# Performance work log

Hardware: AMD Instinct MI355X
Metric: run time of the kernel (lower is better)

Reference implementation:

```python
import jax, jax.numpy as jnp
import numpy as np

H = 8        # heads
DK = 64      # dim_key
L = 64       # rel_pos_length
BN_EPS = 1e-5


def calc_reindexing_tensor(l, Lr):
    # Appendix B (5): band indicator of shape [l, l, 2L-1]
    x = jnp.arange(l)[:, None, None]
    i = jnp.arange(l)[None, :, None]
    r = jnp.arange(-(Lr - 1), Lr)[None, None, :]
    return ((i - x == r) & (jnp.abs(i - x) <= Lr)).astype(jnp.float32)


def setup_inputs() -> dict:
    key = jax.random.key(0)
    ks = jax.random.split(key, 6)
    b, c, x, y = 8, 256, 64, 64
    dim_hidden = H * DK
    return {
        "img": jax.random.normal(ks[0], (b, c, x, y), jnp.float32),
        "w_qkv": jax.random.normal(ks[1], (dim_hidden * 3, c), jnp.float32) * 0.02,
        "w_out": jax.random.normal(ks[2], (c, dim_hidden), jnp.float32) * 0.02,
        "b_out": jnp.zeros((c,), jnp.float32),
        "rel_rows": jax.random.normal(ks[3], (2 * L - 1, DK), jnp.float32),
        "rel_columns": jax.random.normal(ks[4], (2 * L - 1, DK), jnp.float32),
        "bn_gamma": jnp.ones((DK,), jnp.float32),
        "bn_beta": jnp.zeros((DK,), jnp.float32),
    }


def reference(img, w_qkv, w_out, b_out, rel_rows, rel_columns, bn_gamma, bn_beta):
    b, c, x, y = img.shape
    m = x * y
    # 1x1 conv (no bias) == channel GEMM
    qkv = jnp.einsum('bcxy,oc->boxy', img, w_qkv)
    q, k, v = jnp.split(qkv, 3, axis=1)
    # (b, H*DK, x, y) -> (b*H, DK, x*y)
    q = q.reshape(b * H, DK, m)
    k = k.reshape(b * H, DK, m)
    v = v.reshape(b * H, DK, m)

    # linear-attention content path
    k = jax.nn.softmax(k, axis=-1)
    context = jnp.einsum('ndm,nem->nde', k, v)          # (n, DK, DK)
    content_out = jnp.einsum('nde,ndm->nem', context, q)  # norm_queries=False
    content_out = content_out.reshape(b * H, DK, x, y)

    # relative-position path (dense banded einsums, faithful to original)
    q4 = q.reshape(b * H, DK, x, y)
    v4 = v.reshape(b * H, DK, x, y)
    Ix = calc_reindexing_tensor(x, L)                   # (x, x, 2L-1)
    Px = jnp.einsum('xir,rd->xid', Ix, rel_rows)        # (x, x, DK)
    Sx = jnp.einsum('ndxy,xid->nixy', q4, Px)
    Yh = jnp.einsum('nixy,neiy->nexy', Sx, v4)
    # BatchNorm2d(DK), training-mode batch stats over (n, x, y)
    mean = Yh.mean(axis=(0, 2, 3), keepdims=True)
    var = Yh.var(axis=(0, 2, 3), keepdims=True)
    Yh = (Yh - mean) * jax.lax.rsqrt(var + BN_EPS)
    Yh = Yh * bn_gamma[None, :, None, None] + bn_beta[None, :, None, None]

    Iy = Ix if x == y else calc_reindexing_tensor(y, L)
    Py = jnp.einsum('yir,rd->yid', Iy, rel_columns)     # (y, y, DK)
    Sy = jnp.einsum('ndxy,yid->nixy', q4, Py)
    rel_pos_out = jnp.einsum('nixy,nexi->nexy', Sy, Yh)

    out = content_out + rel_pos_out                     # (b*H, DK, x, y)
    out = out.reshape(b, H * DK, x, y)
    # 1x1 conv with bias
    return jnp.einsum('bcxy,oc->boxy', out, w_out) + b_out[None, :, None, None]
```

## Files before the change

### kernel.cpp

```cpp
#include <hip/hip_runtime.h>
#include <hip/hip_bf16.h>
#include <math.h>

#define NH   64
#define DKC  64
#define MM   4096
#define CC   256
#define RRN  127

typedef __hip_bfloat16 bf16;
__device__ __forceinline__ float b2f(bf16 x) { return __bfloat162float(x); }
__device__ __forceinline__ bf16 f2b(float x) { return __float2bfloat16(x); }
__device__ __forceinline__ unsigned short bbits(float x) { bf16 h = f2b(x); return *(unsigned short*)&h; }
__device__ __forceinline__ float fbits(unsigned short u) { bf16 h = *(bf16*)&u; return b2f(h); }

typedef short bf16x8 __attribute__((ext_vector_type(8)));
typedef float f32x4 __attribute__((ext_vector_type(4)));
typedef unsigned short u16;
typedef u16 u16x4 __attribute__((ext_vector_type(4)));
typedef u16 u16x8 __attribute__((ext_vector_type(8)));

#define AS1 __attribute__((address_space(1)))
#define AS3 __attribute__((address_space(3)))
#define GLOAD16(gp, lp) __builtin_amdgcn_global_load_lds((const AS1 void*)(gp), (AS3 void*)(lp), 16, 0, 0)

__device__ __forceinline__ int swzsrc(int lane) { return 8 * ((lane & 7) ^ (lane >> 3)); }
#define FRSWZ(kelem, row) ((kelem) ^ (((row) & 7) * 8))

__global__ __launch_bounds__(256) void k_cvt_all(const float* __restrict__ w_qkv, const float* __restrict__ w_out,
                                                 const float* __restrict__ relc, const float* __restrict__ relr,
                                                 bf16* __restrict__ wb, bf16* __restrict__ wb2,
                                                 bf16* __restrict__ relcb, bf16* __restrict__ relrb) {
  const int i = blockIdx.x * 256 + threadIdx.x;
  if (i < 393216) {
    wb[i] = f2b(w_qkv[i]);
  } else if (i < 524288) {
    int j = i - 393216; wb2[j] = f2b(w_out[j]);
  } else if (i < 532480) {
    int j = i - 524288; relcb[j] = (j < RRN * 64) ? f2b(relc[j]) : f2b(0.f);
  } else {
    int j = i - 532480; if (j < RRN * 64) relrb[j] = f2b(relr[j]);
  }
}

__global__ __launch_bounds__(256) void k_timg(const float* __restrict__ img, bf16* __restrict__ imgT) {
  const int b = blockIdx.z, c0 = blockIdx.y * 64, m0 = blockIdx.x * 64;
  const int tid = threadIdx.x;
  __shared__ short T[64 * 66];
  const float* ib = img + ((size_t)b * CC + c0) * MM + m0;
#pragma unroll
  for (int j = 0; j < 4; ++j) {
    int f4 = j * 256 + tid;
    int cc = f4 >> 4, mm4 = (f4 & 15) * 4;
    f32x4 v = *(const f32x4*)&ib[(size_t)cc * MM + mm4];
#pragma unroll
    for (int k = 0; k < 4; ++k) T[cc * 66 + mm4 + k] = (short)bbits(v[k]);
  }
  __syncthreads();
  bf16* ob = imgT + ((size_t)b * MM + m0) * CC + c0;
#pragma unroll
  for (int j = 0; j < 4; ++j) {
    int f4 = j * 256 + tid;
    int mm = f4 >> 4, cc4 = (f4 & 15) * 4;
    u16x4 pk;
#pragma unroll
    for (int k = 0; k < 4; ++k) pk[k] = (u16)T[(cc4 + k) * 66 + mm];
    *(u16x4*)&ob[(size_t)mm * CC + cc4] = pk;
  }
}

__global__ __launch_bounds__(256) void k_qkv(const bf16* __restrict__ wb, const bf16* __restrict__ imgT,
                                             bf16* __restrict__ qT, bf16* __restrict__ kk, bf16* __restrict__ v) {
  const int bI = blockIdx.z;
  const int o0 = blockIdx.y * 128;
  const int m0 = blockIdx.x * 128;
  const int tid = threadIdx.x;
  const int lane = tid & 63, wid = tid >> 6;
  const int fr = lane & 15;
  const int fq = lane >> 4;
  const int wm = (wid >> 1) * 64, wn = (wid & 1) * 64;

  __shared__ __align__(16) short smem[17408];
  short* As = smem;
  short* Bs = smem + 8192;

  const bf16* iB = imgT + (size_t)bI * MM * CC;

  f32x4 acc[4][4];
#pragma unroll
  for (int mi = 0; mi < 4; ++mi)
#pragma unroll
    for (int ni = 0; ni < 4; ++ni) acc[mi][ni] = (f32x4){0.f, 0.f, 0.f, 0.f};

  const int srow = lane >> 3;
  const int skc = swzsrc(lane);

  for (int kt = 0; kt < 4; ++kt) {
    const int k0 = kt * 64;
#pragma unroll
    for (int cc = 0; cc < 4; ++cc) {
      const int c = wid * 4 + cc;
      const int r = c * 8 + srow;
      GLOAD16(wb + (size_t)(o0 + r) * CC + k0 + skc, &As[c * 512]);
      GLOAD16(iB + (size_t)(m0 + r) * CC + k0 + skc, &Bs[c * 512]);
    }
    __syncthreads();
    bf16x8 af[4][2], bfr[4][2];
#pragma unroll
    for (int mi = 0; mi < 4; ++mi)
#pragma unroll
      for (int kkk = 0; kkk < 2; ++kkk)
        af[mi][kkk] = *(const bf16x8*)&As[(wm + mi * 16 + fr) * 64 + FRSWZ(kkk * 32 + fq * 8, fr)];
#pragma unroll
    for (int ni = 0; ni < 4; ++ni)
#pragma unroll
      for (int kkk = 0; kkk < 2; ++kkk)
        bfr[ni][kkk] = *(const bf16x8*)&Bs[(wn + ni * 16 + fr) * 64 + FRSWZ(kkk * 32 + fq * 8, fr)];
#pragma unroll
    for (int mi = 0; mi < 4; ++mi)
#pragma unroll
      for (int ni = 0; ni < 4; ++ni)
#pragma unroll
        for (int kkk = 0; kkk < 2; ++kkk)
          acc[mi][ni] = __builtin_amdgcn_mfma_f32_16x16x32_bf16(af[mi][kkk], bfr[ni][kkk], acc[mi][ni], 0, 0, 0);
    __syncthreads();
  }

  short* Cs = smem;
  if (o0 < 512) {
#pragma unroll
    for (int mi = 0; mi < 4; ++mi)
#pragma unroll
      for (int ni = 0; ni < 4; ++ni)
#pragma unroll
        for (int r = 0; r < 4; ++r)
          Cs[(wn + ni * 16 + fr) * 136 + wm + mi * 16 + fq * 4 + r] = (short)bbits(acc[mi][ni][r]);
    __syncthreads();
    const int n0 = bI * 8 + (o0 >> 6);
#pragma unroll
    for (int j = 0; j < 8; ++j) {
      int flat = tid + j * 256;
      int m = flat >> 4, nh = (flat >> 3) & 1, ds = flat & 7;
      u16x8 pk = *(const u16x8*)&Cs[m * 136 + nh * 64 + ds * 8];
      *(u16x8*)&qT[((size_t)(n0 + nh) * MM + m0 + m) * 64 + ds * 8] = pk;
    }
  } else {
#pragma unroll
    for (int mi = 0; mi < 4; ++mi)
#pragma unroll
      for (int ni = 0; ni < 4; ++ni)
#pragma unroll
        for (int r = 0; r < 4; ++r)
          Cs[(wm + mi * 16 + fq * 4 + r) * 136 + wn + ni * 16 + fr] = (short)bbits(acc[mi][ni][r]);
    __syncthreads();
    bf16* dst = (o0 < 1024) ? kk : v;
    const int obase = (o0 < 1024) ? (o0 - 512) : (o0 - 1024);
#pragma unroll
    for (int j = 0; j < 8; ++j) {
      int flat = tid + j * 256;
      int row = flat >> 4, seg = flat & 15;
      u16x8 pk = *(const u16x8*)&Cs[row * 136 + seg * 8];
      *(u16x8*)&dst[((size_t)bI * 512 + obase + row) * MM + m0 + seg * 8] = pk;
    }
  }
}

__global__ __launch_bounds__(256) void k_softmax(bf16* __restrict__ kk) {
  const size_t row = blockIdx.x;
  bf16* p = kk + row * (size_t)MM;
  const int t = threadIdx.x;
  __shared__ float sred[4];
  float v[16];
  float mx = -1e30f;
#pragma unroll
  for (int j = 0; j < 4; ++j) {
    u16x4 v4 = *(const u16x4*)&p[(j * 256 + t) * 4];
#pragma unroll
    for (int k = 0; k < 4; ++k) { v[j * 4 + k] = fbits(v4[k]); mx = fmaxf(mx, v[j * 4 + k]); }
  }
#pragma unroll
  for (int off = 32; off; off >>= 1) mx = fmaxf(mx, __shfl_down(mx, off));
  if ((t & 63) == 0) sred[t >> 6] = mx;
  __syncthreads();
  mx = fmaxf(fmaxf(sred[0], sred[1]), fmaxf(sred[2], sred[3]));
  __syncthreads();
  float s = 0.f;
#pragma unroll
  for (int i = 0; i < 16; ++i) { v[i] = expf(v[i] - mx); s += v[i]; }
#pragma unroll
  for (int off = 32; off; off >>= 1) s += __shfl_down(s, off);
  if ((t & 63) == 0) sred[t >> 6] = s;
  __syncthreads();
  s = sred[0] + sred[1] + sred[2] + sred[3];
  const float inv = 1.0f / s;
#pragma unroll
  for (int j = 0; j < 4; ++j) {
    u16x4 o;
#pragma unroll
    for (int k = 0; k < 4; ++k) o[k] = bbits(v[j * 4 + k] * inv);
    *(u16x4*)&p[(j * 256 + t) * 4] = o;
  }
}

__global__ __launch_bounds__(256) void k_ctx2(const bf16* __restrict__ kk, const bf16* __restrict__ v,
                                              float* __restrict__ part) {
  const int ch = blockIdx.x, n = blockIdx.y;
  const int tid = threadIdx.x;
  const int lane = tid & 63, wid = tid >> 6;
  const int fr = lane & 15, fq = lane >> 4;
  const int wr = (wid >> 1) * 32, wc = (wid & 1) * 32;
  __shared__ __align__(16) short Ks[64 * 64];
  __shared__ __align__(16) short Vs[64 * 64];
  const bf16* kp = kk + (size_t)n * DKC * MM;
  const bf16* vp = v + (size_t)n * DKC * MM;
  const int srow = lane >> 3;
  const int skc = swzsrc(lane);

  f32x4 acc[2][2];
#pragma unroll
  for (int mi = 0; mi < 2; ++mi)
#pragma unroll
    for (int ni = 0; ni < 2; ++ni) acc[mi][ni] = (f32x4){0.f, 0.f, 0.f, 0.f};

  for (int t = 0; t < 16; ++t) {
    const int m0 = ch * 1024 + t * 64;
#pragma unroll
    for (int cc = 0; cc < 4; ++cc) {
      const int c = wid * 4 + cc;
      if (c < 8) {
        const int r = c * 8 + srow;
        GLOAD16(kp + (size_t)r * MM + m0 + skc, &Ks[c * 512]);
      } else {
        const int r = (c - 8) * 8 + srow;
        GLOAD16(vp + (size_t)r * MM + m0 + skc, &Vs[(c - 8) * 512]);
      }
    }
    __syncthreads();
    bf16x8 af[2][2], bf[2][2];
#pragma unroll
    for (int mi = 0; mi < 2; ++mi)
#pragma unroll
      for (int kkx = 0; kkx < 2; ++kkx)
        af[mi][kkx] = *(const bf16x8*)&Ks[(wr + mi * 16 + fr) * 64 + FRSWZ(kkx * 32 + fq * 8, fr)];
#pragma unroll
    for (int ni = 0; ni < 2; ++ni)
#pragma unroll
      for (int kkx = 0; kkx < 2; ++kkx)
        bf[ni][kkx] = *(const bf16x8*)&Vs[(wc + ni * 16 + fr) * 64 + FRSWZ(kkx * 32 + fq * 8, fr)];
#pragma unroll
    for (int mi = 0; mi < 2; ++mi)
#pragma unroll
      for (int ni = 0; ni < 2; ++ni)
#pragma unroll
        for (int kkx = 0; kkx < 2; ++kkx)
          acc[mi][ni] = __builtin_amdgcn_mfma_f32_16x16x32_bf16(af[mi][kkx], bf[ni][kkx], acc[mi][ni], 0, 0, 0);
    __syncthreads();
  }
  float* pb = part + ((size_t)ch * NH + n) * 4096;
#pragma unroll
  for (int mi = 0; mi < 2; ++mi)
#pragma unroll
    for (int ni = 0; ni < 2; ++ni)
#pragma unroll
      for (int r = 0; r < 4; ++r)
        pb[(wr + mi * 16 + fq * 4 + r) * 64 + wc + ni * 16 + fr] = acc[mi][ni][r];
}

__global__ __launch_bounds__(256) void k_ctx_red(const float* __restrict__ part, float* __restrict__ ctx) {
  const int idx = blockIdx.x * 256 + threadIdx.x;
  float s = 0.f;
#pragma unroll
  for (int c = 0; c < 4; ++c) s += part[(size_t)c * 262144 + idx];
  ctx[idx] = s;
}

__global__ __launch_bounds__(256) void k_ctxT(const float* __restrict__ ctx, bf16* __restrict__ ctxTb) {
  const int n = blockIdx.x;
  const int tid = threadIdx.x;
  __shared__ float T[64 * 67];
  const float* cn = ctx + (size_t)n * 4096;
#pragma unroll
  for (int l = 0; l < 16; ++l) {
    int idx = tid + l * 256;
    int d = idx >> 6, e = idx & 63;
    T[d * 67 + e] = cn[idx];
  }
  __syncthreads();
  bf16* ob = ctxTb + (size_t)n * 4096;
#pragma unroll
  for (int l = 0; l < 4; ++l) {
    int q = tid + l * 256;
    int e = q >> 4, d4 = (q & 15) * 4;
    u16x4 pk;
#pragma unroll
    for (int k = 0; k < 4; ++k) pk[k] = bbits(T[(d4 + k) * 67 + e]);
    *(u16x4*)&ob[e * 64 + d4] = pk;
  }
}

__global__ __launch_bounds__(256) void k_sx2(const bf16* __restrict__ relrb, const bf16* __restrict__ qT,
                                             bf16* __restrict__ sxT) {
  const int x = blockIdx.x, n = blockIdx.y;
  const int tid = threadIdx.x;
  const int lane = tid & 63, wid = tid >> 6;
  const int fr = lane & 15, fq = lane >> 4;
  const int wr = (wid >> 1) * 32, wc = (wid & 1) * 32;
  __shared__ __align__(16) short Qt[64 * 64];
  const bf16* qrow = qT + ((size_t)n * MM + x * 64) * 64;
  const int srow = lane >> 3, skc = swzsrc(lane);
#pragma unroll
  for (int cc = 0; cc < 2; ++cc) {
    const int c = wid * 2 + cc;
    const int r = c * 8 + srow;
    GLOAD16(qrow + (size_t)r * 64 + skc, &Qt[c * 512]);
  }
  bf16x8 af[2][2];
#pragma unroll
  for (int mi = 0; mi < 2; ++mi) {
    const int j = wr + mi * 16 + fr + 63 - x;
#pragma unroll
    for (int kk = 0; kk < 2; ++kk)
      af[mi][kk] = *(const bf16x8*)&relrb[(size_t)j * 64 + kk * 32 + fq * 8];
  }
  __syncthreads();
  bf16x8 bq[2][2];
#pragma unroll
  for (int ni = 0; ni < 2; ++ni) {
    const int row = wc + ni * 16 + fr;
#pragma unroll
    for (int kk = 0; kk < 2; ++kk)
      bq[ni][kk] = *(const bf16x8*)&Qt[row * 64 + FRSWZ(kk * 32 + fq * 8, fr)];
  }
  f32x4 acc[2][2];
#pragma unroll
  for (int mi = 0; mi < 2; ++mi)
#pragma unroll
    for (int ni = 0; ni < 2; ++ni) acc[mi][ni] = (f32x4){0.f, 0.f, 0.f, 0.f};
#pragma unroll
  for (int mi = 0; mi < 2; ++mi)
#pragma unroll
    for (int ni = 0; ni < 2; ++ni)
#pragma unroll
      for (int kk = 0; kk < 2; ++kk)
        acc[mi][ni] = __builtin_amdgcn_mfma_f32_16x16x32_bf16(af[mi][kk], bq[ni][kk], acc[mi][ni], 0, 0, 0);
#pragma unroll
  for (int mi = 0; mi < 2; ++mi)
#pragma unroll
    for (int ni = 0; ni < 2; ++ni) {
      const int yy2 = wc + ni * 16 + fr;
      u16x4 pk;
#pragma unroll
      for (int r = 0; r < 4; ++r) pk[r] = bbits(acc[mi][ni][r]);
      *(u16x4*)&sxT[(((size_t)n * 64 + yy2) * 64 + x) * 64 + wr + mi * 16 + fq * 4] = pk;
    }
}

__global__ __launch_bounds__(256) void k_vt(const bf16* __restrict__ v, bf16* __restrict__ vT) {
  const int eg = blockIdx.x, n = blockIdx.y;
  const int tid = threadIdx.x;
  __shared__ short T[8 * 64 * 66];
  const bf16* vp = v + (size_t)n * DKC * MM + (size_t)eg * 8 * MM;
#pragma unroll
  for (int j = 0; j < 16; ++j) {
    int flat = (j * 256 + tid) * 8;
    int e = flat >> 12, m = flat & 4095;
    int x = m >> 6, y0 = m & 63;
    u16x4 lo = *(const u16x4*)&vp[(size_t)e * MM + m];
    u16x4 hi = *(const u16x4*)&vp[(size_t)e * MM + m + 4];
#pragma unroll
    for (int k = 0; k < 4; ++k) T[(e * 64 + y0 + k) * 66 + x] = (short)lo[k];
#pragma unroll
    for (int k = 0; k < 4; ++k) T[(e * 64 + y0 + 4 + k) * 66 + x] = (short)hi[k];
  }
  __syncthreads();
#pragma unroll
  for (int j = 0; j < 32; ++j) {
    int flat4 = j * 256 + tid;
    int x4 = flat4 & 15, e = (flat4 >> 4) & 7, y = flat4 >> 7;
    u16x4 pk;
#pragma unroll
    for (int r = 0; r < 4; ++r) pk[r] = (u16)T[(e * 64 + y) * 66 + x4 * 4 + r];
    *(u16x4*)&vT[(((size_t)n * 64 + y) * 64 + eg * 8 + e) * 64 + x4 * 4] = pk;
  }
}

__global__ __launch_bounds__(256) void k_yh2(const bf16* __restrict__ vT, const bf16* __restrict__ sxT,
                                             bf16* __restrict__ yhT) {
  const int y = blockIdx.x, n = blockIdx.y;
  const int tid = threadIdx.x;
  const int lane = tid & 63, wid = tid >> 6;
  const int fr = lane & 15, fq = lane >> 4;
  const int wr = (wid >> 1) * 32, wc = (wid & 1) * 32;
  __shared__ __align__(16) short Va[64 * 64];
  __shared__ __align__(16) short Sa[64 * 64];
  const size_t rb = ((size_t)n * 64 + y) * 4096;
  const int srow = lane >> 3;
  const int skc = swzsrc(lane);
#pragma unroll
  for (int cc = 0; cc < 2; ++cc) {
    const int c = wid * 2 + cc;
    const int r = c * 8 + srow;
    GLOAD16(vT + rb + (size_t)r * 64 + skc, &Va[c * 512]);
    GLOAD16(sxT + rb + (size_t)r * 64 + skc, &Sa[c * 512]);
  }
  __syncthreads();
  bf16x8 av[2][2], bs[2][2];
#pragma unroll
  for (int mi = 0; mi < 2; ++mi)
#pragma unroll
    for (int kk = 0; kk < 2; ++kk)
      av[mi][kk] = *(const bf16x8*)&Va[(wr + mi * 16 + fr) * 64 + FRSWZ(kk * 32 + fq * 8, fr)];
#pragma unroll
  for (int ni = 0; ni < 2; ++ni)
#pragma unroll
    for (int kk = 0; kk < 2; ++kk)
      bs[ni][kk] = *(const bf16x8*)&Sa[(wc + ni * 16 + fr) * 64 + FRSWZ(kk * 32 + fq * 8, fr)];
  f32x4 acc[2][2];
#pragma unroll
  for (int mi = 0; mi < 2; ++mi)
#pragma unroll
    for (int ni = 0; ni < 2; ++ni) acc[mi][ni] = (f32x4){0.f, 0.f, 0.f, 0.f};
#pragma unroll
  for (int mi = 0; mi < 2; ++mi)
#pragma unroll
    for (int ni = 0; ni < 2; ++ni)
#pragma unroll
      for (int kk = 0; kk < 2; ++kk)
        acc[mi][ni] = __builtin_amdgcn_mfma_f32_16x16x32_bf16(av[mi][kk], bs[ni][kk], acc[mi][ni], 0, 0, 0);
#pragma unroll
  for (int mi = 0; mi < 2; ++mi)
#pragma unroll
    for (int ni = 0; ni < 2; ++ni) {
      const int xo = wc + ni * 16 + fr;
      u16x4 pk;
#pragma unroll
      for (int r = 0; r < 4; ++r) pk[r] = bbits(acc[mi][ni][r]);
      *(u16x4*)&yhT[rb + (size_t)xo * 64 + wr + mi * 16 + fq * 4] = pk;
    }
}

__global__ __launch_bounds__(256) void k_bnpart2(const bf16* __restrict__ yhT, float* __restrict__ ps,
                                                 float* __restrict__ ps2) {
  const int gg = blockIdx.x, n = blockIdx.y;
  const int t = threadIdx.x;
  const int eq = (t & 15) * 4, rg = t >> 4;
  const bf16* p = yhT + (size_t)n * 262144 + (size_t)gg * 512 * 64;
  float s[4] = {}, s2[4] = {};
  for (int r = rg; r < 512; r += 16) {
    u16x4 v4 = *(const u16x4*)&p[(size_t)r * 64 + eq];
#pragma unroll
    for (int k = 0; k < 4; ++k) { float x = fbits(v4[k]); s[k] += x; s2[k] += x * x; }
  }
  __shared__ float ls[16][64], ls2[16][64];
#pragma unroll
  for (int k = 0; k < 4; ++k) { ls[rg][eq + k] = s[k]; ls2[rg][eq + k] = s2[k]; }
  __syncthreads();
  if (t < 64) {
    float S = 0.f, S2 = 0.f;
#pragma unroll
    for (int g = 0; g < 16; ++g) { S += ls[g][t]; S2 += ls2[g][t]; }
    ps[t * 512 + n * 8 + gg] = S;
    ps2[t * 512 + n * 8 + gg] = S2;
  }
}

__global__ __launch_bounds__(64) void k_bnfin(const float* __restrict__ ps, const float* __restrict__ ps2,
                                              float* __restrict__ mu, float* __restrict__ rs) {
  const int e = threadIdx.x;
  float S = 0.f, S2 = 0.f;
  for (int g = 0; g < 512; ++g) { S += ps[e * 512 + g]; S2 += ps2[e * 512 + g]; }
  const float invN = 1.0f / (NH * (float)MM);
  float m = S * invN;
  float var = S2 * invN - m * m;
  mu[e] = m;
  rs[e] = 1.0f / sqrtf(var + 1e-5f);
}

__global__ __launch_bounds__(256) void k_crc(const bf16* __restrict__ ctxTb, const bf16* __restrict__ qT,
                                             const bf16* __restrict__ yhT, const bf16* __restrict__ relcb,
                                             const float* __restrict__ mu, const float* __restrict__ rs,
                                             const float* __restrict__ gamma, const float* __restrict__ beta,
                                             bf16* __restrict__ contentT) {
  const int xx = blockIdx.x, n = blockIdx.y;
  const int bI = n >> 3, h = n & 7;
  const int tid = threadIdx.x;
  const int lane = tid & 63, wv = tid >> 6;
  const int fr = lane & 15, fq = lane >> 4;
  __shared__ __align__(16) short smem[4096 + 8448 + 4608];
  short* Qt = smem;
  bf16* Scb = (bf16*)(smem + 4096);
  bf16* Ysb = (bf16*)(smem + 4096 + 8448);
  short* DT = smem;

  const size_t nb = (size_t)n * DKC * MM;

  {
    const bf16* qrow = qT + ((size_t)n * MM + xx * 64) * 64;
    const int srow = lane >> 3, skc = swzsrc(lane);
#pragma unroll
    for (int cc = 0; cc < 2; ++cc) {
      const int c = wv * 2 + cc;
      const int r = c * 8 + srow;
      GLOAD16(qrow + (size_t)r * 64 + skc, &Qt[c * 512]);
    }
  }
#pragma unroll
  for (int l = 0; l < 16; ++l) {
    int idx = tid + l * 256;
    int i = idx >> 6, e = idx & 63;
    float val = (b2f(yhT[nb + (size_t)i * 4096 + xx * 64 + e]) - mu[e]) * rs[e] * gamma[e] + beta[e];
    Ysb[e * 72 + (i ^ (8 * (e >> 3)))] = f2b(val);
  }
  bf16x8 afr[2][2], aCT[2];
#pragma unroll
  for (int mi = 0; mi < 2; ++mi)
#pragma unroll
    for (int kk = 0; kk < 2; ++kk)
      afr[mi][kk] = *(const bf16x8*)&relcb[(size_t)(wv * 32 + mi * 16 + fr) * 64 + kk * 32 + fq * 8];
#pragma unroll
  for (int kk = 0; kk < 2; ++kk)
    aCT[kk] = *(const bf16x8*)&ctxTb[(size_t)n * 4096 + (wv * 16 + fr) * 64 + kk * 32 + fq * 8];
  __syncthreads();

  f32x4 acc1[2][4];
#pragma unroll
  for (int mi = 0; mi < 2; ++mi)
#pragma unroll
    for (int ni = 0; ni < 4; ++ni) acc1[mi][ni] = (f32x4){0.f, 0.f, 0.f, 0.f};
  bf16x8 bq[4][2];
#pragma unroll
  for (int ni = 0; ni < 4; ++ni) {
    const int row = ni * 16 + fr;
#pragma unroll
    for (int kk = 0; kk < 2; ++kk)
      bq[ni][kk] = *(const bf16x8*)&Qt[row * 64 + FRSWZ(kk * 32 + fq * 8, fr)];
  }
#pragma unroll
  for (int mi = 0; mi < 2; ++mi)
#pragma unroll
    for (int ni = 0; ni < 4; ++ni)
#pragma unroll
      for (int kk = 0; kk < 2; ++kk)
        acc1[mi][ni] = __builtin_amdgcn_mfma_f32_16x16x32_bf16(afr[mi][kk], bq[ni][kk], acc1[mi][ni], 0, 0, 0);
#pragma unroll
  for (int mi = 0; mi < 2; ++mi)
#pragma unroll
    for (int ni = 0; ni < 4; ++ni)
#pragma unroll
      for (int r = 0; r < 4; ++r)
        Scb[(wv * 32 + mi * 16 + fq * 4 + r) * 66 + ni * 16 + fr] = f2b(acc1[mi][ni][r]);
  __syncthreads();

#pragma unroll
  for (int l = 0; l < 16; ++l) {
    int idx = tid + l * 256;
    int y = idx >> 6, i = idx & 63;
    DT[y * 64 + FRSWZ(i, y)] = *(const short*)&Scb[(i - y + 63) * 66 + y];
  }
  __syncthreads();

  f32x4 acc2[4];
#pragma unroll
  for (int ni = 0; ni < 4; ++ni) acc2[ni] = (f32x4){0.f, 0.f, 0.f, 0.f};
#pragma unroll
  for (int ni = 0; ni < 4; ++ni)
#pragma unroll
    for (int kk = 0; kk < 2; ++kk)
      acc2[ni] = __builtin_amdgcn_mfma_f32_16x16x32_bf16(aCT[kk], bq[ni][kk], acc2[ni], 0, 0, 0);
  bf16x8 a2[2], bd[4][2];
  {
    const int row = wv * 16 + fr;
    const int swz = 8 * (row >> 3);
#pragma unroll
    for (int kk = 0; kk < 2; ++kk)
      a2[kk] = *(const bf16x8*)&Ysb[row * 72 + ((kk * 32 + fq * 8) ^ swz)];
  }
#pragma unroll
  for (int ni = 0; ni < 4; ++ni) {
    const int row = ni * 16 + fr;
#pragma unroll
    for (int kk = 0; kk < 2; ++kk)
      bd[ni][kk] = *(const bf16x8*)&DT[row * 64 + FRSWZ(kk * 32 + fq * 8, fr)];
  }
#pragma unroll
  for (int ni = 0; ni < 4; ++ni)
#pragma unroll
    for (int kk = 0; kk < 2; ++kk)
      acc2[ni] = __builtin_amdgcn_mfma_f32_16x16x32_bf16(a2[kk], bd[ni][kk], acc2[ni], 0, 0, 0);

  bf16* cb = contentT + (size_t)bI * MM * 512;
#pragma unroll
  for (int ni = 0; ni < 4; ++ni) {
    size_t a = (size_t)(xx * 64 + ni * 16 + fr) * 512 + h * 64 + wv * 16 + fq * 4;
    u16x4 pk;
#pragma unroll
    for (int r = 0; r < 4; ++r) pk[r] = bbits(acc2[ni][r]);
    *(u16x4*)&cb[a] = pk;
  }
}

__global__ __launch_bounds__(256) void k_final(const bf16* __restrict__ wb2, const bf16* __restrict__ cT,
                                               const float* __restrict__ bout, float* __restrict__ dout) {
  const int bI = blockIdx.z;
  const int o0 = blockIdx.y * 128;
  const int m0 = blockIdx.x * 128;
  const int tid = threadIdx.x;
  const int lane = tid & 63, wid = tid >> 6;
  const int fr = lane & 15;
  const int fq = lane >> 4;
  const int wm = (wid >> 1) * 64, wn = (wid & 1) * 64;

  __shared__ __align__(16) short smem[17408];
  short* As = smem;
  short* Bs = smem + 8192;

  const bf16* cB = cT + (size_t)bI * MM * 512;

  f32x4 acc[4][4];
#pragma unroll
  for (int mi = 0; mi < 4; ++mi)
#pragma unroll
    for (int ni = 0; ni < 4; ++ni) acc[mi][ni] = (f32x4){0.f, 0.f, 0.f, 0.f};

  const int srow = lane >> 3;
  const int skc = swzsrc(lane);

  for (int kt = 0; kt < 8; ++kt) {
    const int k0 = kt * 64;
#pragma unroll
    for (int cc = 0; cc < 4; ++cc) {
      const int c = wid * 4 + cc;
      const int r = c * 8 + srow;
      GLOAD16(wb2 + (size_t)(o0 + r) * 512 + k0 + skc, &As[c * 512]);
      GLOAD16(cB + (size_t)(m0 + r) * 512 + k0 + skc, &Bs[c * 512]);
    }
    __syncthreads();
    bf16x8 af[4][2], bfr[4][2];
#pragma unroll
    for (int mi = 0; mi < 4; ++mi)
#pragma unroll
      for (int kkk = 0; kkk < 2; ++kkk)
        af[mi][kkk] = *(const bf16x8*)&As[(wm + mi * 16 + fr) * 64 + FRSWZ(kkk * 32 + fq * 8, fr)];
#pragma unroll
    for (int ni = 0; ni < 4; ++ni)
#pragma unroll
      for (int kkk = 0; kkk < 2; ++kkk)
        bfr[ni][kkk] = *(const bf16x8*)&Bs[(wn + ni * 16 + fr) * 64 + FRSWZ(kkk * 32 + fq * 8, fr)];
#pragma unroll
    for (int mi = 0; mi < 4; ++mi)
#pragma unroll
      for (int ni = 0; ni < 4; ++ni)
#pragma unroll
        for (int kkk = 0; kkk < 2; ++kkk)
          acc[mi][ni] = __builtin_amdgcn_mfma_f32_16x16x32_bf16(af[mi][kkk], bfr[ni][kkk], acc[mi][ni], 0, 0, 0);
    __syncthreads();
  }

  float* Cf = (float*)smem;
#pragma unroll
  for (int half = 0; half < 2; ++half) {
    if ((wm >> 6) == half) {
#pragma unroll
      for (int mi = 0; mi < 4; ++mi)
#pragma unroll
        for (int ni = 0; ni < 4; ++ni)
#pragma unroll
          for (int r = 0; r < 4; ++r) {
            const int rowh = mi * 16 + fq * 4 + r;
            Cf[rowh * 132 + wn + ni * 16 + fr] = acc[mi][ni][r] + bout[o0 + half * 64 + rowh];
          }
    }
    __syncthreads();
#pragma unroll
    for (int j = 0; j < 8; ++j) {
      int flat = tid + j * 256;
      int rowh = flat >> 5, seg = flat & 31;
      f32x4 pk = *(const f32x4*)&Cf[rowh * 132 + seg * 4];
      *(f32x4*)&dout[((size_t)bI * 256 + o0 + half * 64 + rowh) * MM + m0 + seg * 4] = pk;
    }
    __syncthreads();
  }
}

extern "C" void kernel_launch(void* const* d_in, const int* in_sizes, int n_in,
                              void* d_out, int out_size, void* d_ws, size_t ws_size,
                              hipStream_t stream) {
  const float* img = (const float*)d_in[0];
  const float* w_qkv = (const float*)d_in[1];
  const float* w_out = (const float*)d_in[2];
  const float* b_out = (const float*)d_in[3];
  const float* rel_rows = (const float*)d_in[4];
  const float* rel_cols = (const float*)d_in[5];
  const float* gamma = (const float*)d_in[6];
  const float* beta = (const float*)d_in[7];
  float* out = (float*)d_out;

  const size_t SZ = (size_t)NH * DKC * MM;
  bf16* qbuf = (bf16*)d_ws;
  bf16* kbuf = qbuf + SZ;
  bf16* vbuf = kbuf + SZ;
  bf16* imgT = vbuf + SZ;
  float* ctxp = (float*)imgT;
  float* ctx = ctxp + 4 * 262144;
  float* ps = ctx + 262144;
  float* ps2 = ps + 32768;
  float* mu = ps2 + 32768;
  float* rs = mu + 64;
  bf16* wb = imgT + 8388608;
  bf16* sxbuf = wb + 393216;
  bf16* wb2 = sxbuf + SZ;
  bf16* relcb = wb2 + 131072;
  bf16* relrb = relcb + 8192;
  bf16* ctxTb = relrb + 8192;

  k_cvt_all<<<2112, 256, 0, stream>>>(w_qkv, w_out, rel_cols, rel_rows, wb, wb2, relcb, relrb);
  k_timg<<<dim3(64, 4, 8), 256, 0, stream>>>(img, imgT);
  k_qkv<<<dim3(32, 12, 8), 256, 0, stream>>>(wb, imgT, qbuf, kbuf, vbuf);
  k_softmax<<<4096, 256, 0, stream>>>(kbuf);
  k_ctx2<<<dim3(4, 64), 256, 0, stream>>>(kbuf, vbuf, ctxp);
  k_ctx_red<<<1024, 256, 0, stream>>>(ctxp, ctx);
  k_ctxT<<<64, 256, 0, stream>>>(ctx, ctxTb);
  k_sx2<<<dim3(64, 64), 256, 0, stream>>>(relrb, qbuf, sxbuf);
  k_vt<<<dim3(8, 64), 256, 0, stream>>>(vbuf, kbuf);
  k_yh2<<<dim3(64, 64), 256, 0, stream>>>(kbuf, sxbuf, vbuf);
  k_bnpart2<<<dim3(8, 64), 256, 0, stream>>>(vbuf, ps, ps2);
  k_bnfin<<<1, 64, 0, stream>>>(ps, ps2, mu, rs);
  k_crc<<<dim3(64, 64), 256, 0, stream>>>(ctxTb, qbuf, vbuf, relcb, mu, rs, gamma, beta, sxbuf);
  k_final<<<dim3(32, 2, 8), 256, 0, stream>>>(wb2, sxbuf, b_out, out);
}
```

Measured before the change: 200.2 us.

## Double-buffer GEMM LDS tiles, remap blocks across XCDs, fuse context reduce+transpose

```diff
diff --git a/kernel.cpp b/kernel.cpp
--- a/kernel.cpp
+++ b/kernel.cpp
@@ -71,18 +71,19 @@
 
 __global__ __launch_bounds__(256) void k_qkv(const bf16* __restrict__ wb, const bf16* __restrict__ imgT,
                                              bf16* __restrict__ qT, bf16* __restrict__ kk, bf16* __restrict__ v) {
-  const int bI = blockIdx.z;
-  const int o0 = blockIdx.y * 128;
-  const int m0 = blockIdx.x * 128;
+  int flat = blockIdx.x + (blockIdx.y << 5) + blockIdx.z * 384;
+  flat = ((flat & 7) * 384) + (flat >> 3);
+  const int bI = flat / 384;
+  const int r2 = flat - bI * 384;
+  const int o0 = (r2 >> 5) * 128;
+  const int m0 = (r2 & 31) * 128;
   const int tid = threadIdx.x;
   const int lane = tid & 63, wid = tid >> 6;
   const int fr = lane & 15;
   const int fq = lane >> 4;
   const int wm = (wid >> 1) * 64, wn = (wid & 1) * 64;
 
-  __shared__ __align__(16) short smem[17408];
-  short* As = smem;
-  short* Bs = smem + 8192;
+  __shared__ __align__(16) short smem[32768];
 
   const bf16* iB = imgT + (size_t)bI * MM * CC;
 
@@ -95,27 +96,40 @@
   const int srow = lane >> 3;
   const int skc = swzsrc(lane);
 
+#pragma unroll
+  for (int cc = 0; cc < 4; ++cc) {
+    const int c = wid * 4 + cc;
+    const int r = c * 8 + srow;
+    GLOAD16(wb + (size_t)(o0 + r) * CC + skc, &smem[c * 512]);
+    GLOAD16(iB + (size_t)(m0 + r) * CC + skc, &smem[16384 + c * 512]);
+  }
+  __syncthreads();
+
+#pragma unroll
   for (int kt = 0; kt < 4; ++kt) {
-    const int k0 = kt * 64;
-#pragma unroll
-    for (int cc = 0; cc < 4; ++cc) {
-      const int c = wid * 4 + cc;
-      const int r = c * 8 + srow;
-      GLOAD16(wb + (size_t)(o0 + r) * CC + k0 + skc, &As[c * 512]);
-      GLOAD16(iB + (size_t)(m0 + r) * CC + k0 + skc, &Bs[c * 512]);
-    }
-    __syncthreads();
+    const int buf = (kt & 1) * 8192;
+    if (kt < 3) {
+      const int k1 = (kt + 1) * 64;
+      const int nbuf = ((kt + 1) & 1) * 8192;
+#pragma unroll
+      for (int cc = 0; cc < 4; ++cc) {
+        const int c = wid * 4 + cc;
+        const int r = c * 8 + srow;
+        GLOAD16(wb + (size_t)(o0 + r) * CC + k1 + skc, &smem[nbuf + c * 512]);
+        GLOAD16(iB + (size_t)(m0 + r) * CC + k1 + skc, &smem[16384 + nbuf + c * 512]);
+      }
+    }
     bf16x8 af[4][2], bfr[4][2];
 #pragma unroll
     for (int mi = 0; mi < 4; ++mi)
 #pragma unroll
       for (int kkk = 0; kkk < 2; ++kkk)
-        af[mi][kkk] = *(const bf16x8*)&As[(wm + mi * 16 + fr) * 64 + FRSWZ(kkk * 32 + fq * 8, fr)];
+        af[mi][kkk] = *(const bf16x8*)&smem[buf + (wm + mi * 16 + fr) * 64 + FRSWZ(kkk * 32 + fq * 8, fr)];
 #pragma unroll
     for (int ni = 0; ni < 4; ++ni)
 #pragma unroll
       for (int kkk = 0; kkk < 2; ++kkk)
-        bfr[ni][kkk] = *(const bf16x8*)&Bs[(wn + ni * 16 + fr) * 64 + FRSWZ(kkk * 32 + fq * 8, fr)];
+        bfr[ni][kkk] = *(const bf16x8*)&smem[16384 + buf + (wn + ni * 16 + fr) * 64 + FRSWZ(kkk * 32 + fq * 8, fr)];
 #pragma unroll
     for (int mi = 0; mi < 4; ++mi)
 #pragma unroll
@@ -139,8 +153,8 @@
     const int n0 = bI * 8 + (o0 >> 6);
 #pragma unroll
     for (int j = 0; j < 8; ++j) {
-      int flat = tid + j * 256;
-      int m = flat >> 4, nh = (flat >> 3) & 1, ds = flat & 7;
+      int f2 = tid + j * 256;
+      int m = f2 >> 4, nh = (f2 >> 3) & 1, ds = f2 & 7;
       u16x8 pk = *(const u16x8*)&Cs[m * 136 + nh * 64 + ds * 8];
       *(u16x8*)&qT[((size_t)(n0 + nh) * MM + m0 + m) * 64 + ds * 8] = pk;
     }
@@ -157,8 +171,8 @@
     const int obase = (o0 < 1024) ? (o0 - 512) : (o0 - 1024);
 #pragma unroll
     for (int j = 0; j < 8; ++j) {
-      int flat = tid + j * 256;
-      int row = flat >> 4, seg = flat & 15;
+      int f2 = tid + j * 256;
+      int row = f2 >> 4, seg = f2 & 15;
       u16x8 pk = *(const u16x8*)&Cs[row * 136 + seg * 8];
       *(u16x8*)&dst[((size_t)bI * 512 + obase + row) * MM + m0 + seg * 8] = pk;
     }
@@ -266,24 +280,19 @@
         pb[(wr + mi * 16 + fq * 4 + r) * 64 + wc + ni * 16 + fr] = acc[mi][ni][r];
 }
 
-__global__ __launch_bounds__(256) void k_ctx_red(const float* __restrict__ part, float* __restrict__ ctx) {
-  const int idx = blockIdx.x * 256 + threadIdx.x;
-  float s = 0.f;
-#pragma unroll
-  for (int c = 0; c < 4; ++c) s += part[(size_t)c * 262144 + idx];
-  ctx[idx] = s;
-}
-
-__global__ __launch_bounds__(256) void k_ctxT(const float* __restrict__ ctx, bf16* __restrict__ ctxTb) {
+__global__ __launch_bounds__(256) void k_ctxred_T(const float* __restrict__ part, bf16* __restrict__ ctxTb) {
   const int n = blockIdx.x;
   const int tid = threadIdx.x;
   __shared__ float T[64 * 67];
-  const float* cn = ctx + (size_t)n * 4096;
+  const float* pn = part + (size_t)n * 4096;
 #pragma unroll
   for (int l = 0; l < 16; ++l) {
     int idx = tid + l * 256;
     int d = idx >> 6, e = idx & 63;
-    T[d * 67 + e] = cn[idx];
+    float s = 0.f;
+#pragma unroll
+    for (int c = 0; c < 4; ++c) s += pn[(size_t)c * 262144 + idx];
+    T[d * 67 + e] = s;
   }
   __syncthreads();
   bf16* ob = ctxTb + (size_t)n * 4096;
@@ -300,7 +309,9 @@
 
 __global__ __launch_bounds__(256) void k_sx2(const bf16* __restrict__ relrb, const bf16* __restrict__ qT,
                                              bf16* __restrict__ sxT) {
-  const int x = blockIdx.x, n = blockIdx.y;
+  int flat = blockIdx.x + (blockIdx.y << 6);
+  flat = ((flat & 7) * 512) + (flat >> 3);
+  const int x = flat & 63, n = flat >> 6;
   const int tid = threadIdx.x;
   const int lane = tid & 63, wid = tid >> 6;
   const int fr = lane & 15, fq = lane >> 4;
@@ -386,7 +397,9 @@
 
 __global__ __launch_bounds__(256) void k_yh2(const bf16* __restrict__ vT, const bf16* __restrict__ sxT,
                                              bf16* __restrict__ yhT) {
-  const int y = blockIdx.x, n = blockIdx.y;
+  int flat = blockIdx.x + (blockIdx.y << 6);
+  flat = ((flat & 7) * 512) + (flat >> 3);
+  const int y = flat & 63, n = flat >> 6;
   const int tid = threadIdx.x;
   const int lane = tid & 63, wid = tid >> 6;
   const int fr = lane & 15, fq = lane >> 4;
@@ -481,7 +494,9 @@
                                              const float* __restrict__ mu, const float* __restrict__ rs,
                                              const float* __restrict__ gamma, const float* __restrict__ beta,
                                              bf16* __restrict__ contentT) {
-  const int xx = blockIdx.x, n = blockIdx.y;
+  int flat = blockIdx.x + (blockIdx.y << 6);
+  flat = ((flat & 7) * 512) + (flat >> 3);
+  const int xx = flat & 63, n = flat >> 6;
   const int bI = n >> 3, h = n & 7;
   const int tid = threadIdx.x;
   const int lane = tid & 63, wv = tid >> 6;
@@ -601,18 +616,19 @@
 
 __global__ __launch_bounds__(256) void k_final(const bf16* __restrict__ wb2, const bf16* __restrict__ cT,
                                                const float* __restrict__ bout, float* __restrict__ dout) {
-  const int bI = blockIdx.z;
-  const int o0 = blockIdx.y * 128;
-  const int m0 = blockIdx.x * 128;
+  int flat = blockIdx.x + (blockIdx.y << 5) + blockIdx.z * 64;
+  flat = ((flat & 7) * 64) + (flat >> 3);
+  const int bI = flat >> 6;
+  const int r2 = flat & 63;
+  const int o0 = (r2 >> 5) * 128;
+  const int m0 = (r2 & 31) * 128;
   const int tid = threadIdx.x;
   const int lane = tid & 63, wid = tid >> 6;
   const int fr = lane & 15;
   const int fq = lane >> 4;
   const int wm = (wid >> 1) * 64, wn = (wid & 1) * 64;
 
-  __shared__ __align__(16) short smem[17408];
-  short* As = smem;
-  short* Bs = smem + 8192;
+  __shared__ __align__(16) short smem[32768];
 
   const bf16* cB = cT + (size_t)bI * MM * 512;
 
@@ -625,27 +641,39 @@
   const int srow = lane >> 3;
   const int skc = swzsrc(lane);
 
+#pragma unroll
+  for (int cc = 0; cc < 4; ++cc) {
+    const int c = wid * 4 + cc;
+    const int r = c * 8 + srow;
+    GLOAD16(wb2 + (size_t)(o0 + r) * 512 + skc, &smem[c * 512]);
+    GLOAD16(cB + (size_t)(m0 + r) * 512 + skc, &smem[16384 + c * 512]);
+  }
+  __syncthreads();
+
   for (int kt = 0; kt < 8; ++kt) {
-    const int k0 = kt * 64;
-#pragma unroll
-    for (int cc = 0; cc < 4; ++cc) {
-      const int c = wid * 4 + cc;
-      const int r = c * 8 + srow;
-      GLOAD16(wb2 + (size_t)(o0 + r) * 512 + k0 + skc, &As[c * 512]);
-      GLOAD16(cB + (size_t)(m0 + r) * 512 + k0 + skc, &Bs[c * 512]);
-    }
-    __syncthreads();
+    const int buf = (kt & 1) * 8192;
+    if (kt < 7) {
+      const int k1 = (kt + 1) * 64;
+      const int nbuf = ((kt + 1) & 1) * 8192;
+#pragma unroll
+      for (int cc = 0; cc < 4; ++cc) {
+        const int c = wid * 4 + cc;
+        const int r = c * 8 + srow;
+        GLOAD16(wb2 + (size_t)(o0 + r) * 512 + k1 + skc, &smem[nbuf + c * 512]);
+        GLOAD16(cB + (size_t)(m0 + r) * 512 + k1 + skc, &smem[16384 + nbuf + c * 512]);
+      }
+    }
     bf16x8 af[4][2], bfr[4][2];
 #pragma unroll
     for (int mi = 0; mi < 4; ++mi)
 #pragma unroll
       for (int kkk = 0; kkk < 2; ++kkk)
-        af[mi][kkk] = *(const bf16x8*)&As[(wm + mi * 16 + fr) * 64 + FRSWZ(kkk * 32 + fq * 8, fr)];
+        af[mi][kkk] = *(const bf16x8*)&smem[buf + (wm + mi * 16 + fr) * 64 + FRSWZ(kkk * 32 + fq * 8, fr)];
 #pragma unroll
     for (int ni = 0; ni < 4; ++ni)
 #pragma unroll
       for (int kkk = 0; kkk < 2; ++kkk)
-        bfr[ni][kkk] = *(const bf16x8*)&Bs[(wn + ni * 16 + fr) * 64 + FRSWZ(kkk * 32 + fq * 8, fr)];
+        bfr[ni][kkk] = *(const bf16x8*)&smem[16384 + buf + (wn + ni * 16 + fr) * 64 + FRSWZ(kkk * 32 + fq * 8, fr)];
 #pragma unroll
     for (int mi = 0; mi < 4; ++mi)
 #pragma unroll
@@ -673,8 +701,8 @@
     __syncthreads();
 #pragma unroll
     for (int j = 0; j < 8; ++j) {
-      int flat = tid + j * 256;
-      int rowh = flat >> 5, seg = flat & 31;
+      int f2 = tid + j * 256;
+      int rowh = f2 >> 5, seg = f2 & 31;
       f32x4 pk = *(const f32x4*)&Cf[rowh * 132 + seg * 4];
       *(f32x4*)&dout[((size_t)bI * 256 + o0 + half * 64 + rowh) * MM + m0 + seg * 4] = pk;
     }
@@ -718,8 +746,7 @@
   k_qkv<<<dim3(32, 12, 8), 256, 0, stream>>>(wb, imgT, qbuf, kbuf, vbuf);
   k_softmax<<<4096, 256, 0, stream>>>(kbuf);
   k_ctx2<<<dim3(4, 64), 256, 0, stream>>>(kbuf, vbuf, ctxp);
-  k_ctx_red<<<1024, 256, 0, stream>>>(ctxp, ctx);
-  k_ctxT<<<64, 256, 0, stream>>>(ctx, ctxTb);
+  k_ctxred_T<<<64, 256, 0, stream>>>(ctxp, ctxTb);
   k_sx2<<<dim3(64, 64), 256, 0, stream>>>(relrb, qbuf, sxbuf);
   k_vt<<<dim3(8, 64), 256, 0, stream>>>(vbuf, kbuf);
   k_yh2<<<dim3(64, 64), 256, 0, stream>>>(kbuf, sxbuf, vbuf);
```

Result: slower. 204.6 us (+2.2%).
